# Performance work log

Hardware: AMD Instinct MI355X
Metric: run time of the kernel (lower is better)

The kernel has to match this reference:

```python
import jax, jax.numpy as jnp
import numpy as np

EPS_ATTN = 1e-8  # self.eps is undefined in the torch source; standard slot-attention value
LN_EPS = 1e-5


def _ln(x, g=None, b=None, axes=(-1,)):
    m = x.mean(axes, keepdims=True)
    v = ((x - m) ** 2).mean(axes, keepdims=True)
    y = (x - m) * jax.lax.rsqrt(v + LN_EPS)
    return y * g + b if g is not None else y


def setup_inputs() -> dict:
    key = jax.random.key(0)
    ks = jax.random.split(key, 16)
    B, N, S, d, dh = 16, 4096, 8, 64, 128

    def w(k, shape, fan_in):
        return jax.random.normal(k, shape, jnp.float32) / np.float32(np.sqrt(fan_in))

    return {
        "inputs": jax.random.normal(ks[0], (B, N, d + 2), jnp.float32),
        "slots": jax.random.normal(ks[1], (S, d + 4), jnp.float32),
        "Wq": w(ks[2], (d, d), d),
        "Wk": w(ks[3], (d, d), d),
        "Wv": w(ks[4], (d, d), d),
        "Wg": w(ks[5], (d, 2), 2),
        "bg": jnp.zeros((d,), jnp.float32),
        "ln_pos_g": jnp.ones((d,), jnp.float32),
        "ln_pos_b": jnp.zeros((d,), jnp.float32),
        "W1": w(ks[6], (dh, d), d),
        "b1": jnp.zeros((dh,), jnp.float32),
        "W2": w(ks[7], (d, dh), dh),
        "b2": jnp.zeros((d,), jnp.float32),
        "W_ih": w(ks[8], (3 * d, d), d),
        "W_hh": w(ks[9], (3 * d, d), d),
        "b_ih": jnp.zeros((3 * d,), jnp.float32),
        "b_hh": jnp.zeros((3 * d,), jnp.float32),
        "ln_mlp_g": jnp.ones((d,), jnp.float32),
        "ln_mlp_b": jnp.zeros((d,), jnp.float32),
        "W3": w(ks[10], (dh, d), d),
        "b3": jnp.zeros((dh,), jnp.float32),
        "W4": w(ks[11], (d, dh), dh),
        "b4": jnp.zeros((d,), jnp.float32),
        "ln_slot_g": jnp.ones((d,), jnp.float32),
        "ln_slot_b": jnp.zeros((d,), jnp.float32),
        "n_iters": 3,
    }


def reference(inputs, slots, Wq, Wk, Wv, Wg, bg, ln_pos_g, ln_pos_b, W1, b1, W2, b2,
              W_ih, W_hh, b_ih, b_hh, ln_mlp_g, ln_mlp_b, W3, b3, W4, b4,
              ln_slot_g, ln_slot_b, n_iters):
    feats, grids = inputs[..., :-2], inputs[..., -2:]          # (B,N,d), (B,N,2)
    sl, pos, sc = slots[..., :-4], slots[..., -4:-2], slots[..., -2:]
    B, N, _ = feats.shape
    S, d = sl.shape
    scale = d ** (-0.5)

    slots = jnp.broadcast_to(sl, (B, S, d))
    positions = jnp.clip(jnp.broadcast_to(pos, (B, S, 2)), -1.0, 1.0)
    scales = jnp.clip(jnp.broadcast_to(sc, (B, S, 2)), 1e-3, 2.0)

    k = feats @ Wk.T                                           # (B,N,d)
    v = feats @ Wv.T

    def pos_mlp(x):  # LayerNorm -> Linear -> ReLU -> Linear
        h = _ln(x, ln_pos_g, ln_pos_b)
        h = jax.nn.relu(h @ W1.T + b1)
        return h @ W2.T + b2

    for i_iter in range(n_iters + 1):
        rel = (grids[:, :, None] - positions[:, None]) / scales[:, None]  # (B,N,S,2)
        rgp = rel @ Wg.T + bg                                             # (B,N,S,d)
        k_pos = pos_mlp(k[:, :, None] + rgp)                              # (B,N,S,d)
        v_pos = pos_mlp(v[:, :, None] + rgp)

        slots_n = _ln(slots, ln_slot_g, ln_slot_b)
        q = _ln(slots_n, axes=(-2, -1)) @ Wq.T                            # (B,S,d)

        dots = jnp.einsum('bsd,bnsd->bns', q, k_pos) * scale              # (B,N,S)
        attn = jax.nn.softmax(dots, axis=1) + EPS_ATTN
        attn = attn / attn.sum(axis=-1, keepdims=True)

        updates = jnp.einsum('bns,bnsd->bsd', attn, v_pos)                # (B,S,d)
        positions = jnp.einsum('bns,bnp->bsp', attn, grids)               # (B,S,2)
        spread = (grids[:, :, None] - positions[:, None]) ** 2            # (B,N,S,2)
        scales = jnp.clip(jnp.sqrt(jnp.einsum('bns,bnsp->bsp', attn, spread)), 1e-3, 2.0)

        if i_iter < n_iters:
            x = updates.reshape(-1, d)
            h = slots.reshape(-1, d)
            gi = x @ W_ih.T + b_ih
            gh = h @ W_hh.T + b_hh
            i_r, i_z, i_n = jnp.split(gi, 3, axis=-1)
            h_r, h_z, h_n = jnp.split(gh, 3, axis=-1)
            r = jax.nn.sigmoid(i_r + h_r)
            z = jax.nn.sigmoid(i_z + h_z)
            n_g = jnp.tanh(i_n + r * h_n)
            slots = ((1.0 - z) * n_g + z * h).reshape(B, S, d)
            # slot_mlp (no residual in the source)
            hmlp = jax.nn.relu(_ln(slots, ln_mlp_g, ln_mlp_b) @ W3.T + b3)
            slots = hmlp @ W4.T + b4

    return jnp.concatenate([slots, positions, scales], axis=-1)           # (B,S,d+4)
```

## Files before the change

kernel.cpp:

```cpp
#include <hip/hip_runtime.h>
#include <math.h>

#define BB 16
#define NN 4096
#define SS 8
#define DD 64
#define DHH 128
#define CIN 66
#define NITERS 3
#define LN_EPS_F 1e-5f
#define EPS_ATTN_F 1e-8f
#define QSCALE 0.125f
#define LO_SCALE 2048.0f
#define LO_INV 4.8828125e-4f

typedef __attribute__((ext_vector_type(8))) _Float16 half8;
typedef __attribute__((ext_vector_type(4))) float f32x4;
union H8 { half8 v; _Float16 u[8]; };

__device__ __forceinline__ float dot4(float4 a, float4 b) {
    return fmaf(a.x, b.x, fmaf(a.y, b.y, fmaf(a.z, b.z, a.w * b.w)));
}

__device__ __forceinline__ void split_fp16(float z, _Float16& h, _Float16& l) {
    _Float16 hh = (_Float16)z;
    float rem = (z - (float)hh) * LO_SCALE;
    h = hh;
    l = (_Float16)rem;
}

__global__ __launch_bounds__(256) void k_init_slots(
    const float* __restrict__ slots_in, float* __restrict__ slots,
    float* __restrict__ positions, float* __restrict__ scales) {
    int tid = blockIdx.x * 256 + threadIdx.x;
    if (tid < BB * SS * DD) {
        int s = (tid / DD) % SS;
        int c = tid % DD;
        slots[tid] = slots_in[s * 68 + c];
    }
    if (tid < BB * SS * 2) {
        int s = (tid >> 1) & 7;
        int p = tid & 1;
        float po = slots_in[s * 68 + 64 + p];
        positions[tid] = fminf(fmaxf(po, -1.f), 1.f);
        float sc = slots_in[s * 68 + 66 + p];
        scales[tid] = fminf(fmaxf(sc, 1e-3f), 2.f);
    }
}

__global__ __launch_bounds__(256) void k_prep_w(
    const float* __restrict__ W1, const float* __restrict__ lpg,
    const float* __restrict__ lpb, const float* __restrict__ b1,
    const float* __restrict__ Wg,
    float* __restrict__ W1p, float* __restrict__ avec, float* __restrict__ bvec,
    float* __restrict__ s1vec, float* __restrict__ b1p, float* __restrict__ wgc) {
    __shared__ float w1s[128 * 68];
    int tid = threadIdx.x;
    for (int q = 0; q < 8; q++) {
        int flat = q * 1024 + tid * 4;
        int o = flat >> 6, c = flat & 63;
        *(float4*)(w1s + o * 68 + c) = *(const float4*)(W1 + flat);
    }
    __syncthreads();
    if (tid < 128) {
        int o = tid;
        float a = 0.f, bv = 0.f, s1 = 0.f, b1a = b1[o];
        for (int c = 0; c < 64; c++) {
            float w0 = w1s[o * 68 + c];
            float w = w0 * lpg[c];
            W1p[o * 64 + c] = w;
            a = fmaf(w, Wg[2 * c], a);
            bv = fmaf(w, Wg[2 * c + 1], bv);
            s1 += w;
            b1a = fmaf(w0, lpb[c], b1a);
        }
        avec[o] = a; bvec[o] = bv; s1vec[o] = s1; b1p[o] = b1a;
    }
    if (tid == 128) {
        float mwA = 0.f, mwB = 0.f, AA = 0.f, BBv = 0.f, AB = 0.f;
        for (int c = 0; c < 64; c++) {
            float wa = Wg[2 * c], wb = Wg[2 * c + 1];
            mwA += wa; mwB += wb;
            AA = fmaf(wa, wa, AA); BBv = fmaf(wb, wb, BBv); AB = fmaf(wa, wb, AB);
        }
        wgc[0] = mwA * (1.f / 64.f);
        wgc[1] = mwB * (1.f / 64.f);
        wgc[2] = AA * (1.f / 64.f);
        wgc[3] = BBv * (1.f / 64.f);
        wgc[4] = AB * (2.f / 64.f);
    }
}

__global__ __launch_bounds__(256) void k_prep_w2(
    const float* __restrict__ W1p, const float* __restrict__ Wk,
    const float* __restrict__ Wv, const float* __restrict__ bg,
    float* __restrict__ Wall, float* __restrict__ cu) {
    int flat = blockIdx.x * 256 + threadIdx.x;
    int mat = flat >> 13, rem = flat & 8191;
    int o = rem >> 6, c = rem & 63;
    const float* Wm = mat ? Wv : Wk;
    float acc = 0.f;
    for (int d = 0; d < 64; d++)
        acc = fmaf(W1p[o * 64 + d], Wm[d * 64 + c], acc);
    Wall[flat] = acc;
    if (flat < 128) {
        float a = 0.f;
        for (int d = 0; d < 64; d++) a = fmaf(W1p[flat * 64 + d], bg[d], a);
        cu[flat] = a;
    }
}

__global__ __launch_bounds__(256) void k_prep_wT(
    const float* __restrict__ W2, const float* __restrict__ W_ih,
    const float* __restrict__ W_hh, const float* __restrict__ W3,
    const float* __restrict__ W4,
    float* __restrict__ W2T, float* __restrict__ W_ihT,
    float* __restrict__ W_hhT, float* __restrict__ W3T,
    float* __restrict__ W4T) {
    int i = blockIdx.x * 256 + threadIdx.x;
    if (i < 8192) {
        int o = i >> 6, c = i & 63;
        W2T[o * 64 + c] = W2[c * 128 + o];
    } else if (i < 20480) {
        int j = i - 8192;
        int k = j / 192, g = j % 192;
        W_ihT[k * 192 + g] = W_ih[g * 64 + k];
    } else if (i < 32768) {
        int j = i - 20480;
        int k = j / 192, g = j % 192;
        W_hhT[k * 192 + g] = W_hh[g * 64 + k];
    } else if (i < 40960) {
        int j = i - 32768;
        int k = j >> 7, o = j & 127;
        W3T[k * 128 + o] = W3[o * 64 + k];
    } else {
        int j = i - 40960;
        int o = j >> 6, c = j & 63;
        W4T[o * 64 + c] = W4[c * 128 + o];
    }
}

__global__ __launch_bounds__(256) void k_prep_frag(
    const float* __restrict__ Wall, const float* __restrict__ Wk,
    const float* __restrict__ Wv,
    _Float16* __restrict__ cwh, _Float16* __restrict__ cwl,
    _Float16* __restrict__ mwh, _Float16* __restrict__ mwl) {
    int idx = blockIdx.x * 256 + threadIdx.x;
    if (idx < 2048) {
        int f = idx >> 6, lane = idx & 63;
        int m = f >> 4, rest = f & 15;
        int ot = rest >> 1, ks = rest & 1;
        int o = ot * 16 + (lane & 15);
        int k0 = ks * 32 + (lane >> 4) * 8;
        const float* src = Wall + m * 8192 + o * 64 + k0;
        #pragma unroll
        for (int j = 0; j < 8; j++) {
            _Float16 h, l;
            split_fp16(src[j], h, l);
            cwh[(size_t)f * 512 + lane * 8 + j] = h;
            cwl[(size_t)f * 512 + lane * 8 + j] = l;
        }
    } else if (idx < 3072) {
        int id2 = idx - 2048;
        int f = id2 >> 6, lane = id2 & 63;
        int m = f >> 3, rest = f & 7;
        int ot = rest >> 1, ks = rest & 1;
        int o = ot * 16 + (lane & 15);
        int k0 = ks * 32 + (lane >> 4) * 8;
        const float* src = (m ? Wv : Wk) + o * 64 + k0;
        #pragma unroll
        for (int j = 0; j < 8; j++) {
            _Float16 h, l;
            split_fp16(src[j], h, l);
            mwh[(size_t)f * 512 + lane * 8 + j] = h;
            mwl[(size_t)f * 512 + lane * 8 + j] = l;
        }
    }
}

__global__ __launch_bounds__(256) void k_prep_mfma(
    const float* __restrict__ inp,
    const _Float16* __restrict__ cwh, const _Float16* __restrict__ cwl,
    const _Float16* __restrict__ mwh, const _Float16* __restrict__ mwl,
    const float* __restrict__ cu, const float* __restrict__ bg,
    const float* __restrict__ Wg,
    float* __restrict__ uk, float* __restrict__ uv,
    float* __restrict__ kaux, float* __restrict__ vaux, float* __restrict__ gbuf) {
    int tid = threadIdx.x;
    int wv = tid >> 6, lane = tid & 63;
    int quad = lane >> 4, col = lane & 15;
    int mat = blockIdx.y;
    int rowTile = blockIdx.x * 64 + wv * 16;
    half8 ah[2], al[2];
    {
        int rA = rowTile + col;
        const float* rp = inp + (size_t)rA * CIN + quad * 8;
        #pragma unroll
        for (int ks = 0; ks < 2; ks++) {
            H8 h, l;
            #pragma unroll
            for (int q = 0; q < 4; q++) {
                float2 v = *(const float2*)(rp + ks * 32 + 2 * q);
                split_fp16(v.x, h.u[2 * q], l.u[2 * q]);
                split_fp16(v.y, h.u[2 * q + 1], l.u[2 * q + 1]);
            }
            ah[ks] = h.v; al[ks] = l.v;
        }
    }
    const _Float16* cwhm = cwh + (size_t)mat * 16 * 512;
    const _Float16* cwlm = cwl + (size_t)mat * 16 * 512;
    float* dst = mat ? uv : uk;
    float* outb = dst + (size_t)(rowTile + quad * 4) * 128 + col;
    #pragma unroll
    for (int ot = 0; ot < 8; ot++) {
        f32x4 acc1 = {0.f, 0.f, 0.f, 0.f}, acc2 = {0.f, 0.f, 0.f, 0.f};
        #pragma unroll
        for (int ks = 0; ks < 2; ks++) {
            half8 bh = *(const half8*)(cwhm + (size_t)(ot * 2 + ks) * 512 + lane * 8);
            half8 bl = *(const half8*)(cwlm + (size_t)(ot * 2 + ks) * 512 + lane * 8);
            acc1 = __builtin_amdgcn_mfma_f32_16x16x32_f16(ah[ks], bh, acc1, 0, 0, 0);
            acc2 = __builtin_amdgcn_mfma_f32_16x16x32_f16(al[ks], bh, acc2, 0, 0, 0);
            acc2 = __builtin_amdgcn_mfma_f32_16x16x32_f16(ah[ks], bl, acc2, 0, 0, 0);
        }
        float cuv = cu[ot * 16 + col];
        #pragma unroll
        for (int r = 0; r < 4; r++)
            outb[(size_t)r * 128 + ot * 16] = fmaf(acc2[r], LO_INV, acc1[r]) + cuv;
    }
    const _Float16* mwhm = mwh + (size_t)mat * 8 * 512;
    const _Float16* mwlm = mwl + (size_t)mat * 8 * 512;
    float mk[4] = {0.f, 0.f, 0.f, 0.f}, kk2[4] = {0.f, 0.f, 0.f, 0.f};
    float kA[4] = {0.f, 0.f, 0.f, 0.f}, kB[4] = {0.f, 0.f, 0.f, 0.f};
    #pragma unroll
    for (int ot = 0; ot < 4; ot++) {
        f32x4 acc1 = {0.f, 0.f, 0.f, 0.f}, acc2 = {0.f, 0.f, 0.f, 0.f};
        #pragma unroll
        for (int ks = 0; ks < 2; ks++) {
            half8 bh = *(const half8*)(mwhm + (size_t)(ot * 2 + ks) * 512 + lane * 8);
            half8 bl = *(const half8*)(mwlm + (size_t)(ot * 2 + ks) * 512 + lane * 8);
            acc1 = __builtin_amdgcn_mfma_f32_16x16x32_f16(ah[ks], bh, acc1, 0, 0, 0);
            acc2 = __builtin_amdgcn_mfma_f32_16x16x32_f16(al[ks], bh, acc2, 0, 0, 0);
            acc2 = __builtin_amdgcn_mfma_f32_16x16x32_f16(ah[ks], bl, acc2, 0, 0, 0);
        }
        int o = ot * 16 + col;
        float bgo = bg[o], wa = Wg[2 * o], wb = Wg[2 * o + 1];
        #pragma unroll
        for (int r = 0; r < 4; r++) {
            float x = fmaf(acc2[r], LO_INV, acc1[r]) + bgo;
            mk[r] += x; kk2[r] = fmaf(x, x, kk2[r]);
            kA[r] = fmaf(x, wa, kA[r]); kB[r] = fmaf(x, wb, kB[r]);
        }
    }
    #pragma unroll
    for (int off = 1; off <= 8; off <<= 1) {
        #pragma unroll
        for (int r = 0; r < 4; r++) {
            mk[r] += __shfl_xor(mk[r], off, 64);
            kk2[r] += __shfl_xor(kk2[r], off, 64);
            kA[r] += __shfl_xor(kA[r], off, 64);
            kB[r] += __shfl_xor(kB[r], off, 64);
        }
    }
    float* aux = mat ? vaux : kaux;
    if (col == 0) {
        #pragma unroll
        for (int r = 0; r < 4; r++) {
            int row = rowTile + quad * 4 + r;
            float2 g = *(const float2*)(inp + (size_t)row * CIN + 64);
            float4 m1 = {mk[r] * (1.f / 64.f), kk2[r] * (1.f / 64.f),
                         kA[r] * (1.f / 32.f), kB[r] * (1.f / 32.f)};
            float4 m2 = {g.x, g.y, 0.f, 0.f};
            *(float4*)(aux + (size_t)row * 8) = m1;
            *(float4*)(aux + (size_t)row * 8 + 4) = m2;
            if (mat == 0) {
                float2 gw = {g.x, g.y};
                *(float2*)(gbuf + (size_t)row * 2) = gw;
            }
        }
    }
}

__global__ __launch_bounds__(512) void k_slot_prep(
    const float* __restrict__ slots, const float* __restrict__ lsg,
    const float* __restrict__ lsb, const float* __restrict__ Wq,
    const float* __restrict__ W2, const float* __restrict__ b2,
    float* __restrict__ w2q, float* __restrict__ qb2) {
    __shared__ float sn[512];
    __shared__ float qv[SS][64];
    __shared__ float wsum[8], wsum2[8];
    int b = blockIdx.x, t = threadIdx.x;
    int s = t >> 6, c = t & 63;
    float x = slots[(b * SS + s) * DD + c];
    float sum = x;
    for (int off = 32; off; off >>= 1) sum += __shfl_xor(sum, off, 64);
    float m = sum * (1.f / 64.f);
    float dv = x - m;
    float vs = dv * dv;
    for (int off = 32; off; off >>= 1) vs += __shfl_xor(vs, off, 64);
    float y = dv * rsqrtf(vs * (1.f / 64.f) + LN_EPS_F) * lsg[c] + lsb[c];
    float s1 = y, s2 = y * y;
    for (int off = 32; off; off >>= 1) { s1 += __shfl_xor(s1, off, 64); s2 += __shfl_xor(s2, off, 64); }
    if (c == 0) { wsum[s] = s1; wsum2[s] = s2; }
    __syncthreads();
    float ts1 = 0.f, ts2 = 0.f;
    #pragma unroll
    for (int i = 0; i < 8; i++) { ts1 += wsum[i]; ts2 += wsum2[i]; }
    float gm = ts1 * (1.f / 512.f);
    float gv = ts2 * (1.f / 512.f) - gm * gm;
    sn[t] = (y - gm) * rsqrtf(gv + LN_EPS_F);
    __syncthreads();
    float acc = 0.f;
    for (int j4 = 0; j4 < 64; j4 += 4)
        acc += dot4(*(const float4*)&sn[s * 64 + j4], *(const float4*)(Wq + c * 64 + j4));
    qv[s][c] = acc;
    __syncthreads();
    float a0 = 0.f, a1 = 0.f;
    for (int cc = 0; cc < 64; cc++) {
        float qc = qv[s][cc];
        a0 = fmaf(qc, W2[cc * DHH + c], a0);
        a1 = fmaf(qc, W2[cc * DHH + c + 64], a1);
    }
    w2q[(b * SS + s) * DHH + c] = a0 * QSCALE;
    w2q[(b * SS + s) * DHH + c + 64] = a1 * QSCALE;
    float qb = qv[s][c] * b2[c];
    for (int off = 32; off; off >>= 1) qb += __shfl_xor(qb, off, 64);
    if (c == 0) qb2[b * SS + s] = qb * QSCALE;
}

__global__ __launch_bounds__(256) void k_pass1(
    const float* __restrict__ uk, const float* __restrict__ kaux,
    const float* __restrict__ positions, const float* __restrict__ scales,
    const float* __restrict__ avec, const float* __restrict__ bvec,
    const float* __restrict__ s1vec, const float* __restrict__ b1p,
    const float* __restrict__ wgc, const float* __restrict__ w2q,
    const float* __restrict__ qb2, float* __restrict__ dots) {
    int tid = threadIdx.x;
    int chunk = blockIdx.x, b = blockIdx.y;
    int wv = tid >> 6, lane = tid & 63, rh = lane >> 5, ol = lane & 31;
    int o4 = ol * 4;
    float4 a4 = *(const float4*)(avec + o4);
    float4 bv4 = *(const float4*)(bvec + o4);
    float4 s14 = *(const float4*)(s1vec + o4);
    float4 b14 = *(const float4*)(b1p + o4);
    float mwA = wgc[0], mwB = wgc[1], AA = wgc[2], BBc = wgc[3], AB2 = wgc[4];
    float p0[8], p1[8], rc0[8], rc1[8], qb[8];
    float4 wq[8];
    #pragma unroll
    for (int s = 0; s < 8; s++) {
        int bs = b * 8 + s;
        p0[s] = positions[bs * 2]; p1[s] = positions[bs * 2 + 1];
        rc0[s] = 1.f / scales[bs * 2]; rc1[s] = 1.f / scales[bs * 2 + 1];
        qb[s] = qb2[bs];
        wq[s] = *(const float4*)(w2q + (size_t)bs * DHH + o4);
    }
    int row0 = chunk * 64 + wv * 16 + rh;
    size_t rg = (size_t)b * NN + row0;
    float4 m1 = *(const float4*)(kaux + rg * 8);
    float4 m2 = *(const float4*)(kaux + rg * 8 + 4);
    float4 u4 = *(const float4*)(uk + rg * 128 + o4);
    for (int st = 0; st < 8; st++) {
        float4 n1, n2, nu;
        if (st < 7) {
            size_t rgn = rg + (size_t)(st + 1) * 2;
            n1 = *(const float4*)(kaux + rgn * 8);
            n2 = *(const float4*)(kaux + rgn * 8 + 4);
            nu = *(const float4*)(uk + rgn * 128 + o4);
        }
        int row = row0 + st * 2;
        #pragma unroll
        for (int s = 0; s < 8; s++) {
            float rel0 = (m2.x - p0[s]) * rc0[s];
            float rel1 = (m2.y - p1[s]) * rc1[s];
            float m = fmaf(rel1, mwB, fmaf(rel0, mwA, m1.x));
            float q2 = fmaf(rel0, fmaf(rel0, AA, m1.z), m1.y);
            q2 = fmaf(rel1, fmaf(rel1, BBc, m1.w), q2);
            q2 = fmaf(rel0 * rel1, AB2, q2);
            float var = fmaf(-m, m, q2);
            float rstd = rsqrtf(fmaxf(var, 0.f) + LN_EPS_F);
            float p = 0.f, t, h;
            t = fmaf(-m, s14.x, u4.x); t = fmaf(rel0, a4.x, t); t = fmaf(rel1, bv4.x, t);
            h = fmaf(rstd, t, b14.x); p = fmaf(fmaxf(h, 0.f), wq[s].x, p);
            t = fmaf(-m, s14.y, u4.y); t = fmaf(rel0, a4.y, t); t = fmaf(rel1, bv4.y, t);
            h = fmaf(rstd, t, b14.y); p = fmaf(fmaxf(h, 0.f), wq[s].y, p);
            t = fmaf(-m, s14.z, u4.z); t = fmaf(rel0, a4.z, t); t = fmaf(rel1, bv4.z, t);
            h = fmaf(rstd, t, b14.z); p = fmaf(fmaxf(h, 0.f), wq[s].z, p);
            t = fmaf(-m, s14.w, u4.w); t = fmaf(rel0, a4.w, t); t = fmaf(rel1, bv4.w, t);
            h = fmaf(rstd, t, b14.w); p = fmaf(fmaxf(h, 0.f), wq[s].w, p);
            p += __shfl_xor(p, 1, 64);
            p += __shfl_xor(p, 2, 64);
            p += __shfl_xor(p, 4, 64);
            p += __shfl_xor(p, 8, 64);
            p += __shfl_xor(p, 16, 64);
            if (ol == 0)
                dots[(size_t)(b * 8 + s) * NN + row] = p + qb[s];
        }
        m1 = n1; m2 = n2; u4 = nu;
    }
}

__global__ __launch_bounds__(256) void k_pass2(
    const float* __restrict__ uv, const float* __restrict__ vaux,
    const float* __restrict__ positions, const float* __restrict__ scales,
    const float* __restrict__ avec, const float* __restrict__ bvec,
    const float* __restrict__ s1vec, const float* __restrict__ b1p,
    const float* __restrict__ wgc, const float* __restrict__ dots,
    const float* __restrict__ Mv, const float* __restrict__ Lv,
    float* __restrict__ H, float* __restrict__ sacc) {
    __shared__ float Hw[4 * 1024];
    __shared__ float red2[4][8][5];
    int tid = threadIdx.x;
    int chunk = blockIdx.x, b = blockIdx.y;
    int wv = tid >> 6, lane = tid & 63, rh = lane >> 5, ol = lane & 31;
    int o4 = ol * 4;
    float4 a4 = *(const float4*)(avec + o4);
    float4 bv4 = *(const float4*)(bvec + o4);
    float4 s14 = *(const float4*)(s1vec + o4);
    float4 b14 = *(const float4*)(b1p + o4);
    float mwA = wgc[0], mwB = wgc[1], AA = wgc[2], BBc = wgc[3], AB2 = wgc[4];
    float p0[8], p1[8], rc0[8], rc1[8], Ms[8], Li[8];
    #pragma unroll
    for (int s = 0; s < 8; s++) {
        int bs = b * 8 + s;
        p0[s] = positions[bs * 2]; p1[s] = positions[bs * 2 + 1];
        rc0[s] = 1.f / scales[bs * 2]; rc1[s] = 1.f / scales[bs * 2 + 1];
        Ms[s] = Mv[bs]; Li[s] = 1.f / Lv[bs];
    }
    float hq[8][4];
    #pragma unroll
    for (int s = 0; s < 8; s++)
        #pragma unroll
        for (int c = 0; c < 4; c++) hq[s][c] = 0.f;
    float sv0 = 0.f, sv1 = 0.f, sv2 = 0.f, sv3 = 0.f, sv4 = 0.f;
    int row0 = chunk * 64 + wv * 16 + rh;
    size_t rg = (size_t)b * NN + row0;
    float4 m1 = *(const float4*)(vaux + rg * 8);
    float4 m2 = *(const float4*)(vaux + rg * 8 + 4);
    float4 u4 = *(const float4*)(uv + rg * 128 + o4);
    for (int st = 0; st < 8; st++) {
        float4 n1, n2, nu;
        if (st < 7) {
            size_t rgn = rg + (size_t)(st + 1) * 2;
            n1 = *(const float4*)(vaux + rgn * 8);
            n2 = *(const float4*)(vaux + rgn * 8 + 4);
            nu = *(const float4*)(uv + rgn * 128 + o4);
        }
        int row = row0 + st * 2;
        float a[8], rs = 0.f;
        #pragma unroll
        for (int s = 0; s < 8; s++) {
            float d = dots[(size_t)(b * 8 + s) * NN + row];
            a[s] = __expf(d - Ms[s]) * Li[s] + EPS_ATTN_F;
            rs += a[s];
        }
        float inv = 1.f / rs;
        float gx = m2.x, gy = m2.y;
        #pragma unroll
        for (int s = 0; s < 8; s++) {
            float ar = a[s] * inv;
            float apv = (ol == s) ? ar : 0.f;
            sv0 += apv;
            sv1 = fmaf(apv, gx, sv1);
            sv2 = fmaf(apv, gy, sv2);
            sv3 = fmaf(apv, gx * gx, sv3);
            sv4 = fmaf(apv, gy * gy, sv4);
            float rel0 = (gx - p0[s]) * rc0[s];
            float rel1 = (gy - p1[s]) * rc1[s];
            float m = fmaf(rel1, mwB, fmaf(rel0, mwA, m1.x));
            float q2 = fmaf(rel0, fmaf(rel0, AA, m1.z), m1.y);
            q2 = fmaf(rel1, fmaf(rel1, BBc, m1.w), q2);
            q2 = fmaf(rel0 * rel1, AB2, q2);
            float var = fmaf(-m, m, q2);
            float rstd = rsqrtf(fmaxf(var, 0.f) + LN_EPS_F);
            float t, h;
            t = fmaf(-m, s14.x, u4.x); t = fmaf(rel0, a4.x, t); t = fmaf(rel1, bv4.x, t);
            h = fmaf(rstd, t, b14.x); hq[s][0] = fmaf(ar, fmaxf(h, 0.f), hq[s][0]);
            t = fmaf(-m, s14.y, u4.y); t = fmaf(rel0, a4.y, t); t = fmaf(rel1, bv4.y, t);
            h = fmaf(rstd, t, b14.y); hq[s][1] = fmaf(ar, fmaxf(h, 0.f), hq[s][1]);
            t = fmaf(-m, s14.z, u4.z); t = fmaf(rel0, a4.z, t); t = fmaf(rel1, bv4.z, t);
            h = fmaf(rstd, t, b14.z); hq[s][2] = fmaf(ar, fmaxf(h, 0.f), hq[s][2]);
            t = fmaf(-m, s14.w, u4.w); t = fmaf(rel0, a4.w, t); t = fmaf(rel1, bv4.w, t);
            h = fmaf(rstd, t, b14.w); hq[s][3] = fmaf(ar, fmaxf(h, 0.f), hq[s][3]);
        }
        m1 = n1; m2 = n2; u4 = nu;
    }
    #pragma unroll
    for (int s = 0; s < 8; s++)
        #pragma unroll
        for (int c = 0; c < 4; c++)
            hq[s][c] += __shfl_xor(hq[s][c], 32, 64);
    sv0 += __shfl_xor(sv0, 32, 64);
    sv1 += __shfl_xor(sv1, 32, 64);
    sv2 += __shfl_xor(sv2, 32, 64);
    sv3 += __shfl_xor(sv3, 32, 64);
    sv4 += __shfl_xor(sv4, 32, 64);
    if (lane < 32) {
        #pragma unroll
        for (int s = 0; s < 8; s++) {
            float4 st = {hq[s][0], hq[s][1], hq[s][2], hq[s][3]};
            *(float4*)(Hw + wv * 1024 + s * 128 + o4) = st;
        }
    }
    if (lane < 8) {
        red2[wv][lane][0] = sv0;
        red2[wv][lane][1] = sv1;
        red2[wv][lane][2] = sv2;
        red2[wv][lane][3] = sv3;
        red2[wv][lane][4] = sv4;
    }
    __syncthreads();
    #pragma unroll
    for (int q = 0; q < 4; q++) {
        int flat = q * 256 + tid;
        float sum = Hw[flat] + Hw[1024 + flat] + Hw[2048 + flat] + Hw[3072 + flat];
        atomicAdd(&H[(size_t)b * 8 * DHH + flat], sum);
    }
    if (tid < 40) {
        int s = tid / 5, j = tid % 5;
        float sum = red2[0][s][j] + red2[1][s][j] + red2[2][s][j] + red2[3][s][j];
        atomicAdd(&sacc[(b * 8 + s) * 8 + j], sum);
    }
}

__global__ __launch_bounds__(256) void k_softmax_ms(
    const float* __restrict__ dots, float* __restrict__ Mv, float* __restrict__ Lv,
    float* __restrict__ H, float* __restrict__ sacc) {
    __shared__ float red[4];
    int bs = blockIdx.x, t = threadIdx.x;
    if (t < 128) H[(size_t)bs * DHH + t] = 0.f;
    if (t < 8) sacc[bs * 8 + t] = 0.f;
    const float* dp = dots + (size_t)bs * NN;
    float mx = -1e30f;
    #pragma unroll
    for (int it = 0; it < 4; it++) {
        float4 d = *(const float4*)(dp + it * 1024 + t * 4);
        mx = fmaxf(mx, fmaxf(fmaxf(d.x, d.y), fmaxf(d.z, d.w)));
    }
    for (int off = 32; off; off >>= 1) mx = fmaxf(mx, __shfl_xor(mx, off, 64));
    if ((t & 63) == 0) red[t >> 6] = mx;
    __syncthreads();
    float M = fmaxf(fmaxf(red[0], red[1]), fmaxf(red[2], red[3]));
    __syncthreads();
    float sm = 0.f;
    #pragma unroll
    for (int it = 0; it < 4; it++) {
        float4 d = *(const float4*)(dp + it * 1024 + t * 4);
        sm += __expf(d.x - M) + __expf(d.y - M) + __expf(d.z - M) + __expf(d.w - M);
    }
    for (int off = 32; off; off >>= 1) sm += __shfl_xor(sm, off, 64);
    if ((t & 63) == 0) red[t >> 6] = sm;
    __syncthreads();
    if (t == 0) { Mv[bs] = M; Lv[bs] = red[0] + red[1] + red[2] + red[3]; }
}

__global__ __launch_bounds__(256) void k_stats_only(
    const float* __restrict__ dots, const float* __restrict__ Mv,
    const float* __restrict__ Lv, const float* __restrict__ gbuf,
    float* __restrict__ sacc) {
    __shared__ float red[4][40];
    int chunk = blockIdx.x, b = blockIdx.y;
    int t = threadIdx.x;
    int n = chunk * 256 + t;
    float2 g = *(const float2*)(gbuf + (size_t)(b * NN + n) * 2);
    float gx2 = g.x * g.x, gy2 = g.y * g.y;
    float a[8];
    float rs = 0.f;
    #pragma unroll
    for (int s = 0; s < 8; s++) {
        int bs = b * 8 + s;
        float d = dots[(size_t)bs * NN + n];
        a[s] = __expf(d - Mv[bs]) * (1.f / Lv[bs]) + EPS_ATTN_F;
        rs += a[s];
    }
    float inv = 1.f / rs;
    float v[8][5];
    #pragma unroll
    for (int s = 0; s < 8; s++) {
        float av = a[s] * inv;
        v[s][0] = av;
        v[s][1] = av * g.x;  v[s][2] = av * g.y;
        v[s][3] = av * gx2;  v[s][4] = av * gy2;
    }
    #pragma unroll
    for (int off = 1; off <= 32; off <<= 1)
        #pragma unroll
        for (int s = 0; s < 8; s++)
            #pragma unroll
            for (int j = 0; j < 5; j++)
                v[s][j] += __shfl_xor(v[s][j], off, 64);
    int lane = t & 63, wv = t >> 6;
    if (lane == 0) {
        #pragma unroll
        for (int s = 0; s < 8; s++)
            #pragma unroll
            for (int j = 0; j < 5; j++)
                red[wv][s * 5 + j] = v[s][j];
    }
    __syncthreads();
    if (t < 40) {
        float sum = red[0][t] + red[1][t] + red[2][t] + red[3][t];
        int s = t / 5, j = t % 5;
        atomicAdd(&sacc[(b * 8 + s) * 8 + j], sum);
    }
}

__global__ __launch_bounds__(64) void k_gru_mlp(
    const float* __restrict__ H, const float* __restrict__ sacc,
    const float* __restrict__ W2T, const float* __restrict__ b2,
    const float* __restrict__ W_ihT, const float* __restrict__ W_hhT,
    const float* __restrict__ b_ih, const float* __restrict__ b_hh,
    const float* __restrict__ lmg, const float* __restrict__ lmb,
    const float* __restrict__ W3T, const float* __restrict__ b3,
    const float* __restrict__ W4T, const float* __restrict__ b4,
    float* __restrict__ slots, float* __restrict__ positions,
    float* __restrict__ scales) {
    int bs = blockIdx.x;
    int c = threadIdx.x;
    __shared__ float hl[DHH], ul[DD], sl[DD], yl[DD], hml[DHH];
    float A0 = sacc[bs * 8 + 0];
    if (c < 2) {
        float A1 = sacc[bs * 8 + 1 + c];
        float A2 = sacc[bs * 8 + 3 + c];
        positions[bs * 2 + c] = A1;
        float sx = A2 - A1 * A1 * (2.f - A0);
        scales[bs * 2 + c] = fminf(fmaxf(sqrtf(fmaxf(sx, 0.f)), 1e-3f), 2.f);
    }
    hl[c] = H[bs * DHH + c];
    hl[c + 64] = H[bs * DHH + 64 + c];
    float hold = slots[bs * DD + c];
    sl[c] = hold;
    __syncthreads();
    float u = A0 * b2[c];
    #pragma unroll 8
    for (int o = 0; o < DHH; o++)
        u = fmaf(W2T[o * 64 + c], hl[o], u);
    ul[c] = u;
    __syncthreads();
    float gir = b_ih[c], giz = b_ih[64 + c], gin = b_ih[128 + c];
    float ghr = b_hh[c], ghz = b_hh[64 + c], ghn = b_hh[128 + c];
    #pragma unroll 4
    for (int k = 0; k < DD; k++) {
        float uu = ul[k], hh = sl[k];
        const float* wi = W_ihT + k * 192 + c;
        const float* wh = W_hhT + k * 192 + c;
        gir = fmaf(uu, wi[0], gir);
        giz = fmaf(uu, wi[64], giz);
        gin = fmaf(uu, wi[128], gin);
        ghr = fmaf(hh, wh[0], ghr);
        ghz = fmaf(hh, wh[64], ghz);
        ghn = fmaf(hh, wh[128], ghn);
    }
    float rg = 1.f / (1.f + __expf(-(gir + ghr)));
    float zg = 1.f / (1.f + __expf(-(giz + ghz)));
    float ng = tanhf(gin + rg * ghn);
    float snew = (1.f - zg) * ng + zg * hold;
    float sum = snew;
    for (int off = 32; off; off >>= 1) sum += __shfl_xor(sum, off, 64);
    float m = sum * (1.f / 64.f);
    float dv = snew - m;
    float vv = dv * dv;
    for (int off = 32; off; off >>= 1) vv += __shfl_xor(vv, off, 64);
    yl[c] = dv * rsqrtf(vv * (1.f / 64.f) + LN_EPS_F) * lmg[c] + lmb[c];
    __syncthreads();
    float h0 = b3[c], h1 = b3[64 + c];
    #pragma unroll 4
    for (int k = 0; k < DD; k++) {
        float yy = yl[k];
        const float* w3 = W3T + k * 128 + c;
        h0 = fmaf(yy, w3[0], h0);
        h1 = fmaf(yy, w3[64], h1);
    }
    hml[c] = fmaxf(h0, 0.f);
    hml[64 + c] = fmaxf(h1, 0.f);
    __syncthreads();
    float outv = b4[c];
    #pragma unroll 8
    for (int o = 0; o < DHH; o++)
        outv = fmaf(hml[o], W4T[o * 64 + c], outv);
    slots[bs * DD + c] = outv;
}

__global__ __launch_bounds__(256) void k_write_out(
    const float* __restrict__ slots, const float* __restrict__ sacc,
    float* __restrict__ out) {
    int tid = blockIdx.x * 256 + threadIdx.x;
    if (tid >= BB * SS * 68) return;
    int bs = tid / 68, c = tid % 68;
    float v;
    if (c < 64) {
        v = slots[bs * 64 + c];
    } else if (c < 66) {
        v = sacc[bs * 8 + 1 + (c - 64)];
    } else {
        int p = c - 66;
        float A0 = sacc[bs * 8 + 0];
        float A1 = sacc[bs * 8 + 1 + p];
        float A2 = sacc[bs * 8 + 3 + p];
        float sx = A2 - A1 * A1 * (2.f - A0);
        v = fminf(fmaxf(sqrtf(fmaxf(sx, 0.f)), 1e-3f), 2.f);
    }
    out[tid] = v;
}

extern "C" void kernel_launch(void* const* d_in, const int* in_sizes, int n_in,
                              void* d_out, int out_size, void* d_ws, size_t ws_size,
                              hipStream_t stream) {
    (void)in_sizes; (void)n_in; (void)out_size; (void)ws_size;
    const float* inp = (const float*)d_in[0];
    const float* slots_in = (const float*)d_in[1];
    const float* Wq = (const float*)d_in[2];
    const float* Wk = (const float*)d_in[3];
    const float* Wv = (const float*)d_in[4];
    const float* Wg = (const float*)d_in[5];
    const float* bg = (const float*)d_in[6];
    const float* lpg = (const float*)d_in[7];
    const float* lpb = (const float*)d_in[8];
    const float* W1 = (const float*)d_in[9];
    const float* b1 = (const float*)d_in[10];
    const float* W2 = (const float*)d_in[11];
    const float* b2 = (const float*)d_in[12];
    const float* W_ih = (const float*)d_in[13];
    const float* W_hh = (const float*)d_in[14];
    const float* b_ih = (const float*)d_in[15];
    const float* b_hh = (const float*)d_in[16];
    const float* lmg = (const float*)d_in[17];
    const float* lmb = (const float*)d_in[18];
    const float* W3 = (const float*)d_in[19];
    const float* b3 = (const float*)d_in[20];
    const float* W4 = (const float*)d_in[21];
    const float* b4 = (const float*)d_in[22];
    const float* lsg = (const float*)d_in[23];
    const float* lsb = (const float*)d_in[24];
    float* out = (float*)d_out;
    float* ws = (float*)d_ws;

    const size_t NR = (size_t)BB * NN;
    size_t o_uk = 0;
    size_t o_uv = o_uk + NR * 128;
    size_t o_kaux = o_uv + NR * 128;
    size_t o_vaux = o_kaux + NR * 8;
    size_t o_gbuf = o_vaux + NR * 8;
    size_t o_dots = o_gbuf + NR * 2;
    size_t o_slots = o_dots + NR * SS;
    size_t o_pos = o_slots + BB * SS * DD;
    size_t o_scl = o_pos + BB * SS * 2;
    size_t o_w2q = o_scl + BB * SS * 2;
    size_t o_qb2 = o_w2q + BB * SS * DHH;
    size_t o_Mv = o_qb2 + BB * SS;
    size_t o_Lv = o_Mv + BB * SS;
    size_t o_H = o_Lv + BB * SS;
    size_t o_sacc = o_H + BB * SS * DHH;
    size_t o_W1p = o_sacc + BB * SS * 8;
    size_t o_avec = o_W1p + DHH * DD;
    size_t o_bvec = o_avec + DHH;
    size_t o_s1v = o_bvec + DHH;
    size_t o_b1p = o_s1v + DHH;
    size_t o_wgc = o_b1p + DHH;
    size_t o_Wall = o_wgc + 8;
    size_t o_cu = o_Wall + 2 * DHH * DD;
    size_t o_cwh = o_cu + DHH;
    size_t o_cwl = o_cwh + 8192;
    size_t o_mwh = o_cwl + 8192;
    size_t o_mwl = o_mwh + 4096;
    size_t o_W2T = o_mwl + 4096;
    size_t o_ihT = o_W2T + 8192;
    size_t o_hhT = o_ihT + 12288;
    size_t o_W3T = o_hhT + 12288;
    size_t o_W4T = o_W3T + 8192;

    float* uk = ws + o_uk;
    float* uv = ws + o_uv;
    float* kaux = ws + o_kaux;
    float* vaux = ws + o_vaux;
    float* gbuf = ws + o_gbuf;
    float* dots = ws + o_dots;
    float* slots = ws + o_slots;
    float* positions = ws + o_pos;
    float* scales = ws + o_scl;
    float* w2q = ws + o_w2q;
    float* qb2 = ws + o_qb2;
    float* Mv = ws + o_Mv;
    float* Lv = ws + o_Lv;
    float* H = ws + o_H;
    float* sacc = ws + o_sacc;
    float* W1p = ws + o_W1p;
    float* avec = ws + o_avec;
    float* bvec = ws + o_bvec;
    float* s1v = ws + o_s1v;
    float* b1p = ws + o_b1p;
    float* wgc = ws + o_wgc;
    float* Wall = ws + o_Wall;
    float* cu = ws + o_cu;
    _Float16* cwh = (_Float16*)(ws + o_cwh);
    _Float16* cwl = (_Float16*)(ws + o_cwl);
    _Float16* mwh = (_Float16*)(ws + o_mwh);
    _Float16* mwl = (_Float16*)(ws + o_mwl);
    float* W2T = ws + o_W2T;
    float* W_ihT = ws + o_ihT;
    float* W_hhT = ws + o_hhT;
    float* W3T = ws + o_W3T;
    float* W4T = ws + o_W4T;

    k_init_slots<<<32, 256, 0, stream>>>(slots_in, slots, positions, scales);
    k_prep_wT<<<192, 256, 0, stream>>>(W2, W_ih, W_hh, W3, W4,
                                       W2T, W_ihT, W_hhT, W3T, W4T);
    k_prep_w<<<1, 256, 0, stream>>>(W1, lpg, lpb, b1, Wg, W1p, avec, bvec, s1v, b1p, wgc);
    k_prep_w2<<<64, 256, 0, stream>>>(W1p, Wk, Wv, bg, Wall, cu);
    k_prep_frag<<<12, 256, 0, stream>>>(Wall, Wk, Wv, cwh, cwl, mwh, mwl);
    k_prep_mfma<<<dim3(1024, 2), 256, 0, stream>>>(inp, cwh, cwl, mwh, mwl,
                                                   cu, bg, Wg, uk, uv, kaux, vaux, gbuf);

    for (int it = 0; it <= NITERS; ++it) {
        k_slot_prep<<<BB, 512, 0, stream>>>(slots, lsg, lsb, Wq, W2, b2, w2q, qb2);
        k_pass1<<<dim3(64, BB), 256, 0, stream>>>(uk, kaux, positions, scales,
                                                  avec, bvec, s1v, b1p, wgc, w2q, qb2, dots);
        k_softmax_ms<<<BB * SS, 256, 0, stream>>>(dots, Mv, Lv, H, sacc);
        if (it < NITERS) {
            k_pass2<<<dim3(64, BB), 256, 0, stream>>>(uv, vaux, positions, scales,
                                                      avec, bvec, s1v, b1p, wgc,
                                                      dots, Mv, Lv, H, sacc);
            k_gru_mlp<<<BB * SS, 64, 0, stream>>>(H, sacc, W2T, b2, W_ihT, W_hhT,
                                                  b_ih, b_hh, lmg, lmb, W3T, b3,
                                                  W4T, b4, slots, positions, scales);
        } else {
            k_stats_only<<<dim3(16, BB), 256, 0, stream>>>(dots, Mv, Lv, gbuf, sacc);
        }
    }
    k_write_out<<<34, 256, 0, stream>>>(slots, sacc, out);
}
```

Baseline: 486.2 us.

## Precompute normalized attention in stats kernel and simplify pass2 to consume it

Moves the softmax normalization and the position/scale statistic accumulation out of pass2 into a separate k_attn_stats kernel that now runs every iteration and writes a normalized attention buffer. Pass2 then reads the precomputed attention instead of recomputing exp, the row sums and the per-slot reductions for every output lane, and drops its shared-memory reduction and sacc atomics. It also adds a min-blocks-per-CU hint of 2 to pass1 and pass2. In exchange it adds an extra kernel launch per iteration plus an extra global write and read of an attention array the size of dots.

```diff
diff --git a/kernel.cpp b/kernel.cpp
--- a/kernel.cpp
+++ b/kernel.cpp
@@ -327,7 +327,7 @@
     if (c == 0) qb2[b * SS + s] = qb * QSCALE;
 }
 
-__global__ __launch_bounds__(256) void k_pass1(
+__global__ __launch_bounds__(256, 2) void k_pass1(
     const float* __restrict__ uk, const float* __restrict__ kaux,
     const float* __restrict__ positions, const float* __restrict__ scales,
     const float* __restrict__ avec, const float* __restrict__ bvec,
@@ -398,16 +398,14 @@
     }
 }
 
-__global__ __launch_bounds__(256) void k_pass2(
+__global__ __launch_bounds__(256, 2) void k_pass2(
     const float* __restrict__ uv, const float* __restrict__ vaux,
     const float* __restrict__ positions, const float* __restrict__ scales,
     const float* __restrict__ avec, const float* __restrict__ bvec,
     const float* __restrict__ s1vec, const float* __restrict__ b1p,
-    const float* __restrict__ wgc, const float* __restrict__ dots,
-    const float* __restrict__ Mv, const float* __restrict__ Lv,
-    float* __restrict__ H, float* __restrict__ sacc) {
+    const float* __restrict__ wgc, const float* __restrict__ attn,
+    float* __restrict__ H) {
     __shared__ float Hw[4 * 1024];
-    __shared__ float red2[4][8][5];
     int tid = threadIdx.x;
     int chunk = blockIdx.x, b = blockIdx.y;
     int wv = tid >> 6, lane = tid & 63, rh = lane >> 5, ol = lane & 31;
@@ -417,20 +415,18 @@
     float4 s14 = *(const float4*)(s1vec + o4);
     float4 b14 = *(const float4*)(b1p + o4);
     float mwA = wgc[0], mwB = wgc[1], AA = wgc[2], BBc = wgc[3], AB2 = wgc[4];
-    float p0[8], p1[8], rc0[8], rc1[8], Ms[8], Li[8];
+    float p0[8], p1[8], rc0[8], rc1[8];
     #pragma unroll
     for (int s = 0; s < 8; s++) {
         int bs = b * 8 + s;
         p0[s] = positions[bs * 2]; p1[s] = positions[bs * 2 + 1];
         rc0[s] = 1.f / scales[bs * 2]; rc1[s] = 1.f / scales[bs * 2 + 1];
-        Ms[s] = Mv[bs]; Li[s] = 1.f / Lv[bs];
     }
     float hq[8][4];
     #pragma unroll
     for (int s = 0; s < 8; s++)
         #pragma unroll
         for (int c = 0; c < 4; c++) hq[s][c] = 0.f;
-    float sv0 = 0.f, sv1 = 0.f, sv2 = 0.f, sv3 = 0.f, sv4 = 0.f;
     int row0 = chunk * 64 + wv * 16 + rh;
     size_t rg = (size_t)b * NN + row0;
     float4 m1 = *(const float4*)(vaux + rg * 8);
@@ -445,26 +441,11 @@
             nu = *(const float4*)(uv + rgn * 128 + o4);
         }
         int row = row0 + st * 2;
-        float a[8], rs = 0.f;
         #pragma unroll
         for (int s = 0; s < 8; s++) {
-            float d = dots[(size_t)(b * 8 + s) * NN + row];
-            a[s] = __expf(d - Ms[s]) * Li[s] + EPS_ATTN_F;
-            rs += a[s];
-        }
-        float inv = 1.f / rs;
-        float gx = m2.x, gy = m2.y;
-        #pragma unroll
-        for (int s = 0; s < 8; s++) {
-            float ar = a[s] * inv;
-            float apv = (ol == s) ? ar : 0.f;
-            sv0 += apv;
-            sv1 = fmaf(apv, gx, sv1);
-            sv2 = fmaf(apv, gy, sv2);
-            sv3 = fmaf(apv, gx * gx, sv3);
-            sv4 = fmaf(apv, gy * gy, sv4);
-            float rel0 = (gx - p0[s]) * rc0[s];
-            float rel1 = (gy - p1[s]) * rc1[s];
+            float ar = attn[(size_t)(b * 8 + s) * NN + row];
+            float rel0 = (m2.x - p0[s]) * rc0[s];
+            float rel1 = (m2.y - p1[s]) * rc1[s];
             float m = fmaf(rel1, mwB, fmaf(rel0, mwA, m1.x));
             float q2 = fmaf(rel0, fmaf(rel0, AA, m1.z), m1.y);
             q2 = fmaf(rel1, fmaf(rel1, BBc, m1.w), q2);
@@ -488,24 +469,12 @@
         #pragma unroll
         for (int c = 0; c < 4; c++)
             hq[s][c] += __shfl_xor(hq[s][c], 32, 64);
-    sv0 += __shfl_xor(sv0, 32, 64);
-    sv1 += __shfl_xor(sv1, 32, 64);
-    sv2 += __shfl_xor(sv2, 32, 64);
-    sv3 += __shfl_xor(sv3, 32, 64);
-    sv4 += __shfl_xor(sv4, 32, 64);
     if (lane < 32) {
         #pragma unroll
         for (int s = 0; s < 8; s++) {
             float4 st = {hq[s][0], hq[s][1], hq[s][2], hq[s][3]};
             *(float4*)(Hw + wv * 1024 + s * 128 + o4) = st;
         }
-    }
-    if (lane < 8) {
-        red2[wv][lane][0] = sv0;
-        red2[wv][lane][1] = sv1;
-        red2[wv][lane][2] = sv2;
-        red2[wv][lane][3] = sv3;
-        red2[wv][lane][4] = sv4;
     }
     __syncthreads();
     #pragma unroll
@@ -513,11 +482,6 @@
         int flat = q * 256 + tid;
         float sum = Hw[flat] + Hw[1024 + flat] + Hw[2048 + flat] + Hw[3072 + flat];
         atomicAdd(&H[(size_t)b * 8 * DHH + flat], sum);
-    }
-    if (tid < 40) {
-        int s = tid / 5, j = tid % 5;
-        float sum = red2[0][s][j] + red2[1][s][j] + red2[2][s][j] + red2[3][s][j];
-        atomicAdd(&sacc[(b * 8 + s) * 8 + j], sum);
     }
 }
 
@@ -552,10 +516,10 @@
     if (t == 0) { Mv[bs] = M; Lv[bs] = red[0] + red[1] + red[2] + red[3]; }
 }
 
-__global__ __launch_bounds__(256) void k_stats_only(
+__global__ __launch_bounds__(256) void k_attn_stats(
     const float* __restrict__ dots, const float* __restrict__ Mv,
     const float* __restrict__ Lv, const float* __restrict__ gbuf,
-    float* __restrict__ sacc) {
+    float* __restrict__ attn, float* __restrict__ sacc) {
     __shared__ float red[4][40];
     int chunk = blockIdx.x, b = blockIdx.y;
     int t = threadIdx.x;
@@ -576,6 +540,7 @@
     #pragma unroll
     for (int s = 0; s < 8; s++) {
         float av = a[s] * inv;
+        attn[(size_t)(b * 8 + s) * NN + n] = av;
         v[s][0] = av;
         v[s][1] = av * g.x;  v[s][2] = av * g.y;
         v[s][3] = av * gx2;  v[s][4] = av * gy2;
@@ -740,7 +705,8 @@
     size_t o_vaux = o_kaux + NR * 8;
     size_t o_gbuf = o_vaux + NR * 8;
     size_t o_dots = o_gbuf + NR * 2;
-    size_t o_slots = o_dots + NR * SS;
+    size_t o_attn = o_dots + NR * SS;
+    size_t o_slots = o_attn + NR * SS;
     size_t o_pos = o_slots + BB * SS * DD;
     size_t o_scl = o_pos + BB * SS * 2;
     size_t o_w2q = o_scl + BB * SS * 2;
@@ -773,6 +739,7 @@
     float* vaux = ws + o_vaux;
     float* gbuf = ws + o_gbuf;
     float* dots = ws + o_dots;
+    float* attn = ws + o_attn;
     float* slots = ws + o_slots;
     float* positions = ws + o_pos;
     float* scales = ws + o_scl;
@@ -814,15 +781,13 @@
         k_pass1<<<dim3(64, BB), 256, 0, stream>>>(uk, kaux, positions, scales,
                                                   avec, bvec, s1v, b1p, wgc, w2q, qb2, dots);
         k_softmax_ms<<<BB * SS, 256, 0, stream>>>(dots, Mv, Lv, H, sacc);
+        k_attn_stats<<<dim3(16, BB), 256, 0, stream>>>(dots, Mv, Lv, gbuf, attn, sacc);
         if (it < NITERS) {
             k_pass2<<<dim3(64, BB), 256, 0, stream>>>(uv, vaux, positions, scales,
-                                                      avec, bvec, s1v, b1p, wgc,
-                                                      dots, Mv, Lv, H, sacc);
+                                                      avec, bvec, s1v, b1p, wgc, attn, H);
             k_gru_mlp<<<BB * SS, 64, 0, stream>>>(H, sacc, W2T, b2, W_ihT, W_hhT,
                                                   b_ih, b_hh, lmg, lmb, W3T, b3,
                                                   W4T, b4, slots, positions, scales);
-        } else {
-            k_stats_only<<<dim3(16, BB), 256, 0, stream>>>(dots, Mv, Lv, gbuf, sacc);
         }
     }
     k_write_out<<<34, 256, 0, stream>>>(slots, sacc, out);
```

Result: faster. 475.3 us (-2.2%).
